# Kernel tuning notes

Measured on AMD Instinct MI355X. Metric: run time of the kernel, lower is better.

## Reference

```python
import jax, jax.numpy as jnp
import numpy as np

B, L, D, H, NL = 16, 256, 768, 12, 4
HD = D // H          # head size = 64; also edge-feature embedding dim
V, E, C, F = 30000, 50, 2, 3072
CLS_ID = 1


def _pos_emb(length, dim):
    # standard sinusoidal positional embedding [L, D]
    pos = jnp.arange(length, dtype=jnp.float32)[:, None]
    div = jnp.exp(-np.log(10000.0) * jnp.arange(0, dim, 2, dtype=jnp.float32) / dim)
    ang = pos * div[None, :]
    pe = jnp.zeros((length, dim), jnp.float32)
    return pe.at[:, 0::2].set(jnp.sin(ang)).at[:, 1::2].set(jnp.cos(ang))


def _ln(x, g, b, eps=1e-5):
    m = x.mean(-1, keepdims=True)
    v = x.var(-1, keepdims=True)
    return (x - m) * jax.lax.rsqrt(v + eps) * g + b


def setup_inputs() -> dict:
    key = jax.random.key(0)
    ks = jax.random.split(key, 16)
    s = 0.02
    word_ids = jax.random.randint(ks[0], (B, L), 0, V).at[:, 0].set(CLS_ID)
    batched_adj = jax.random.bernoulli(ks[1], 0.3, (B, L, L)) | jnp.eye(L, dtype=bool)[None]
    edge_types = jax.random.randint(ks[2], (B, L, L), 0, E)
    word_emb = (jax.random.normal(ks[3], (V, D)) * s).at[0].set(0.0)   # padding_idx=0
    edge_emb = (jax.random.normal(ks[4], (E, HD)) * s).at[0].set(0.0)  # padding_idx=0
    pw = lambda k, shp: jax.random.normal(k, shp) * s
    return {
        "word_ids": word_ids, "batched_adj": batched_adj, "edge_types": edge_types,
        "word_emb": word_emb, "edge_emb": edge_emb,
        "Wq": pw(ks[5], (NL, D, D)), "bq": jnp.zeros((NL, D)),
        "Wk": pw(ks[6], (NL, D, D)), "bk": jnp.zeros((NL, D)),
        "Wv": pw(ks[7], (NL, D, D)), "bv": jnp.zeros((NL, D)),
        "Wo": pw(ks[8], (NL, D, D)), "bo": jnp.zeros((NL, D)),
        "ln1_g": jnp.ones((NL, D)), "ln1_b": jnp.zeros((NL, D)),
        "W1": pw(ks[9], (NL, D, F)), "b1": jnp.zeros((NL, F)),
        "W2": pw(ks[10], (NL, F, D)), "b2": jnp.zeros((NL, D)),
        "ln2_g": jnp.ones((NL, D)), "ln2_b": jnp.zeros((NL, D)),
        "cls_W": pw(ks[11], (D, C)), "cls_b": jnp.zeros((C,)),
    }


def reference(word_ids, batched_adj, edge_types, word_emb, edge_emb,
              Wq, bq, Wk, bk, Wv, bv, Wo, bo, ln1_g, ln1_b,
              W1, b1, W2, b2, ln2_g, ln2_b, cls_W, cls_b):
    # node features: word embedding + positional embedding
    h = word_emb[word_ids] + _pos_emb(L, D)[None]          # [B,L,D]
    scale = 1.0 / np.sqrt(HD)
    eemb = edge_emb[edge_types]                             # [B,L,L,HD] edge key features
    neg = jnp.asarray(-1e9, h.dtype)
    mask = batched_adj[:, None]                             # [B,1,L,L]
    for l in range(NL):
        q = (h @ Wq[l] + bq[l]).reshape(B, L, H, HD)
        k = (h @ Wk[l] + bk[l]).reshape(B, L, H, HD)
        v = (h @ Wv[l] + bv[l]).reshape(B, L, H, HD)
        # scores: node-node + query . edge-key-feature, adjacency-masked
        scores = jnp.einsum('bihd,bjhd->bhij', q, k)
        scores = scores + jnp.einsum('bihd,bijd->bhij', q, eemb)
        scores = jnp.where(mask, scores * scale, neg)
        att = jax.nn.softmax(scores, axis=-1)               # [B,H,L,L]
        out = jnp.einsum('bhij,bjhd->bihd', att, v).reshape(B, L, D)
        h = _ln(h + (out @ Wo[l] + bo[l]), ln1_g[l], ln1_b[l])
        ff = jax.nn.relu(h @ W1[l] + b1[l]) @ W2[l] + b2[l]
        h = _ln(h + ff, ln2_g[l], ln2_b[l])
    cls_h = h[:, 0]                                         # CLS pooling
    logits = cls_h @ cls_W + cls_b                          # [B,C]
    return logits
```

## Files before the change

### kernel.cpp

```cpp
#include <hip/hip_runtime.h>
#include <hip/hip_bf16.h>

#define BB 16
#define LL 256
#define DD 768
#define HH 12
#define HDD 64
#define NLL 4
#define FF 3072
#define EE 50
#define QKVS 2304
#define TOKD ((size_t)BB * LL * DD)

typedef unsigned short ushort_t;
typedef __bf16 bf16x8 __attribute__((ext_vector_type(8)));
typedef float f32x4 __attribute__((ext_vector_type(4)));

__device__ __forceinline__ float b2f(ushort_t u) {
    union { unsigned int i; float f; } x; x.i = ((unsigned int)u) << 16; return x.f;
}
__device__ __forceinline__ ushort_t f2b(float f) {
    unsigned int u = __builtin_bit_cast(unsigned int, f);
    unsigned int r = u + 0x7fffu + ((u >> 16) & 1u);
    return (ushort_t)(r >> 16);
}

__device__ __forceinline__ void gl2lds16(const void* g, void* l) {
    __builtin_amdgcn_global_load_lds(
        (const __attribute__((address_space(1))) unsigned int*)g,
        (__attribute__((address_space(3))) unsigned int*)l,
        16, 0, 0);
}

__global__ __launch_bounds__(256) void transpose_f2b(
    const float* __restrict__ in, ushort_t* __restrict__ out, int R, int C,
    long inZ, long outZ)
{
    __shared__ ushort_t tile[32][33];
    in  += (long)blockIdx.z * inZ;
    out += (long)blockIdx.z * outZ;
    int c0 = blockIdx.x * 32, r0 = blockIdx.y * 32;
    int tx = threadIdx.x, ty = threadIdx.y;
#pragma unroll
    for (int i = 0; i < 32; i += 8)
        tile[ty + i][tx] = f2b(in[(long)(r0 + ty + i) * C + c0 + tx]);
    __syncthreads();
#pragma unroll
    for (int i = 0; i < 32; i += 8)
        out[(long)(c0 + ty + i) * R + r0 + tx] = tile[tx][ty + i];
}

__global__ __launch_bounds__(256) void fuse_bias_kernel(
    const float* __restrict__ bq, const float* __restrict__ bk,
    const float* __restrict__ bv, int l, float* __restrict__ out)
{
    int n = blockIdx.x * 256 + threadIdx.x;
    if (n >= QKVS) return;
    float v = (n < DD) ? bq[l * DD + n]
            : (n < 2 * DD) ? bk[l * DD + n - DD]
            : bv[l * DD + n - 2 * DD];
    out[n] = v;
}

__global__ __launch_bounds__(256) void embed_kernel(
    const int* __restrict__ wids, const float* __restrict__ wemb,
    float* __restrict__ hf, ushort_t* __restrict__ hb)
{
    long idx = (long)blockIdx.x * 256 + threadIdx.x;
    int d = (int)(idx % DD);
    int t = (int)(idx / DD);
    int lpos = t & (LL - 1);
    int wid = wids[t];
    float freq = expf(-9.210340371976184f * (float)(d & ~1) * (1.f / (float)DD));
    float ang = (float)lpos * freq;
    float pe = (d & 1) ? cosf(ang) : sinf(ang);
    float hv = wemb[(long)wid * DD + d] + pe;
    hf[idx] = hv;
    hb[idx] = f2b(hv);
}

__global__ __launch_bounds__(256) void gemm_bf16(
    const ushort_t* __restrict__ A, const ushort_t* __restrict__ Bt,
    const float* __restrict__ bias,
    ushort_t* __restrict__ outb, float* __restrict__ outf,
    int M, int N, int K, int Ksl, int relu)
{
    __shared__ __align__(16) ushort_t As[128 * 32];
    __shared__ __align__(16) ushort_t Bs[128 * 32];
    const int tid = threadIdx.x;
    const int wave = tid >> 6, lane = tid & 63;
    const int quad = lane >> 4, l16 = lane & 15;
    const int m0 = blockIdx.y * 128, n0 = blockIdx.x * 128;
    const int z = blockIdx.z;
    const int kbase = z * Ksl;
    const int wm = (wave >> 1) * 64, wn = (wave & 1) * 64;
    const ushort_t* Ab = A + (long)m0 * K;
    const ushort_t* Bb = Bt + (long)n0 * K;

    f32x4 acc[4][4];
#pragma unroll
    for (int mi = 0; mi < 4; ++mi)
#pragma unroll
        for (int ni = 0; ni < 4; ++ni) acc[mi][ni] = (f32x4){0.f, 0.f, 0.f, 0.f};

    const int nk = Ksl >> 5;
    for (int kt = 0; kt < nk; ++kt) {
        const int k0 = kbase + (kt << 5);
        __syncthreads();
#pragma unroll
        for (int i = 0; i < 2; ++i) {
            int c = tid + i * 256;
            int row = c >> 2, kc = (c & 3) * 8;
            char* la = (char*)As + (wave * 1024 + i * 4096);
            char* lb = (char*)Bs + (wave * 1024 + i * 4096);
            gl2lds16(&Ab[(long)row * K + k0 + kc], la);
            gl2lds16(&Bb[(long)row * K + k0 + kc], lb);
        }
        __syncthreads();
        bf16x8 af[4], bfr[4];
#pragma unroll
        for (int t = 0; t < 4; ++t)
            af[t] = *(const bf16x8*)&As[(wm + t * 16 + l16) * 32 + quad * 8];
#pragma unroll
        for (int t = 0; t < 4; ++t)
            bfr[t] = *(const bf16x8*)&Bs[(wn + t * 16 + l16) * 32 + quad * 8];
#pragma unroll
        for (int mi = 0; mi < 4; ++mi)
#pragma unroll
            for (int ni = 0; ni < 4; ++ni)
                acc[mi][ni] = __builtin_amdgcn_mfma_f32_16x16x32_bf16(
                    af[mi], bfr[ni], acc[mi][ni], 0, 0, 0);
    }

    float* outfz = outf ? outf + (size_t)z * M * N : nullptr;
#pragma unroll
    for (int ni = 0; ni < 4; ++ni) {
        int col = n0 + wn + ni * 16 + l16;
        float bv = (bias && z == 0) ? bias[col] : 0.f;
#pragma unroll
        for (int mi = 0; mi < 4; ++mi) {
#pragma unroll
            for (int r = 0; r < 4; ++r) {
                int row = m0 + wm + mi * 16 + quad * 4 + r;
                float vv = acc[mi][ni][r] + bv;
                if (relu) vv = fmaxf(vv, 0.f);
                if (outb) outb[(long)row * N + col] = f2b(vv);
                if (outfz) outfz[(long)row * N + col] = vv;
            }
        }
    }
}

#define QS_STR 72
#define VT_STR 264
#define P_STR  264
#define S_STR  257
#define PE_STR 53

__global__ __launch_bounds__(256) void attn_kernel(
    const ushort_t* __restrict__ qkv,
    const int* __restrict__ adjm, const int* __restrict__ etyp,
    const float* __restrict__ eemb, ushort_t* __restrict__ out)
{
    __shared__ __align__(16) char smem[64448];
    ushort_t* VT = (ushort_t*)smem;
    float*    S  = (float*)(smem + 33792);
    ushort_t* P  = (ushort_t*)(smem + 50240);
    float*    Pe = (float*)(smem + 58688);
    char*     U  = smem + 62080;
    float* invrow = (float*)(smem + 64384);
    ushort_t* Qs = (ushort_t*)U;
    float*    red = (float*)U;

    const int blk = blockIdx.x;
    const int qt = blk & 15;
    const int h  = (blk >> 4) % HH;
    const int b  = blk / (16 * HH);
    const int i0 = qt * 16;
    const int tid = threadIdx.x;
    const int wave = tid >> 6, lane = tid & 63;
    const int quad = lane >> 4, l16 = lane & 15;

    if (tid < 128) {
        int row = tid >> 3, d0 = (tid & 7) * 8;
        *(int4*)&Qs[row * QS_STR + d0] =
            *(const int4*)&qkv[((long)(b * LL + i0 + row)) * QKVS + h * HDD + d0];
    }
#pragma unroll
    for (int i = 0; i < 8; ++i) {
        int c = tid + i * 256;
        int j = c >> 3, d0 = (c & 7) * 8;
        int4 raw = *(const int4*)&qkv[((long)(b * LL + j)) * QKVS + 2 * DD + h * HDD + d0];
        const ushort_t* vals = (const ushort_t*)&raw;
#pragma unroll
        for (int u = 0; u < 8; ++u) VT[(d0 + u) * VT_STR + j] = vals[u];
    }
    __syncthreads();

    {
        int e = wave * 16 + l16;
        f32x4 acc = (f32x4){0.f, 0.f, 0.f, 0.f};
#pragma unroll
        for (int kk = 0; kk < 2; ++kk) {
            bf16x8 af = *(const bf16x8*)&Qs[l16 * QS_STR + kk * 32 + quad * 8];
            bf16x8 bf = (bf16x8){0, 0, 0, 0, 0, 0, 0, 0};
            if (e < EE) {
                const float* ep = &eemb[(long)e * HDD + kk * 32 + quad * 8];
#pragma unroll
                for (int u = 0; u < 8; ++u) bf[u] = (__bf16)ep[u];
            }
            acc = __builtin_amdgcn_mfma_f32_16x16x32_bf16(af, bf, acc, 0, 0, 0);
        }
        if (e < EE) {
#pragma unroll
            for (int r = 0; r < 4; ++r) Pe[(quad * 4 + r) * PE_STR + e] = acc[r];
        }
    }

#pragma unroll
    for (int jt = 0; jt < 4; ++jt) {
        int jtile = wave * 4 + jt;
        int j = jtile * 16 + l16;
        f32x4 acc = (f32x4){0.f, 0.f, 0.f, 0.f};
#pragma unroll
        for (int kk = 0; kk < 2; ++kk) {
            bf16x8 af = *(const bf16x8*)&Qs[l16 * QS_STR + kk * 32 + quad * 8];
            bf16x8 bf = *(const bf16x8*)&qkv[((long)(b * LL + j)) * QKVS + DD + h * HDD + kk * 32 + quad * 8];
            acc = __builtin_amdgcn_mfma_f32_16x16x32_bf16(af, bf, acc, 0, 0, 0);
        }
#pragma unroll
        for (int r = 0; r < 4; ++r)
            S[(quad * 4 + r) * S_STR + jtile * 16 + l16] = acc[r];
    }
    __syncthreads();

    {
        const int row = tid & 15, seg = tid >> 4;
        const int i = i0 + row;
        const int* etp = etyp + ((long)(b * LL + i)) * LL + seg * 16;
        const int* adp = adjm + ((long)(b * LL + i)) * LL + seg * 16;
        int etv[16], adv[16];
#pragma unroll
        for (int t = 0; t < 4; ++t) {
            *(int4*)&etv[t * 4] = *(const int4*)&etp[t * 4];
            *(int4*)&adv[t * 4] = *(const int4*)&adp[t * 4];
        }
        float vals[16];
        float pmax = -1e30f;
#pragma unroll
        for (int c = 0; c < 16; ++c) {
            float s = S[row * S_STR + seg * 16 + c];
            float pe = Pe[row * PE_STR + etv[c]];
            float vv = adv[c] ? (s + pe) * 0.125f : -1e30f;
            vals[c] = vv;
            pmax = fmaxf(pmax, vv);
        }
        red[row * 17 + seg] = pmax;
        __syncthreads();
        float m = -1e30f;
#pragma unroll
        for (int g = 0; g < 16; ++g) m = fmaxf(m, red[row * 17 + g]);
        float sum = 0.f;
#pragma unroll
        for (int c = 0; c < 16; ++c) {
            float p = __expf(vals[c] - m);
            ushort_t pb = f2b(p);
            sum += b2f(pb);
            P[row * P_STR + seg * 16 + c] = pb;
        }
        red[272 + row * 17 + seg] = sum;
        __syncthreads();
        if (tid < 16) {
            float tot = 0.f;
#pragma unroll
            for (int g = 0; g < 16; ++g) tot += red[272 + tid * 17 + g];
            invrow[tid] = 1.f / tot;
        }
        __syncthreads();
    }

    {
        f32x4 acc = (f32x4){0.f, 0.f, 0.f, 0.f};
#pragma unroll
        for (int kt = 0; kt < 8; ++kt) {
            bf16x8 af = *(const bf16x8*)&P[l16 * P_STR + kt * 32 + quad * 8];
            bf16x8 bf = *(const bf16x8*)&VT[(wave * 16 + l16) * VT_STR + kt * 32 + quad * 8];
            acc = __builtin_amdgcn_mfma_f32_16x16x32_bf16(af, bf, acc, 0, 0, 0);
        }
#pragma unroll
        for (int r = 0; r < 4; ++r) {
            int row = quad * 4 + r;
            float ov = acc[r] * invrow[row];
            out[((long)(b * LL + i0 + row)) * DD + h * HDD + wave * 16 + l16] = f2b(ov);
        }
    }
}

__global__ __launch_bounds__(256) void ln_kernel(
    float* __restrict__ hf, ushort_t* __restrict__ hb,
    const float* __restrict__ proj, int nparts,
    const float* __restrict__ g, const float* __restrict__ be)
{
    const int r = blockIdx.x, tid = threadIdx.x;
    const long rb = (long)r * DD;
    float x[3];
#pragma unroll
    for (int i = 0; i < 3; ++i) {
        int d = tid + i * 256;
        float t = hf[rb + d];
        for (int p = 0; p < nparts; ++p) t += proj[(size_t)p * TOKD + rb + d];
        x[i] = t;
    }
    float s = x[0] + x[1] + x[2];
    float s2 = x[0] * x[0] + x[1] * x[1] + x[2] * x[2];
#pragma unroll
    for (int o = 1; o < 64; o <<= 1) { s += __shfl_xor(s, o); s2 += __shfl_xor(s2, o); }
    __shared__ float rs[4], rq[4];
    int wave = tid >> 6;
    if ((tid & 63) == 0) { rs[wave] = s; rq[wave] = s2; }
    __syncthreads();
    float S  = rs[0] + rs[1] + rs[2] + rs[3];
    float S2 = rq[0] + rq[1] + rq[2] + rq[3];
    float mean = S * (1.f / (float)DD);
    float var  = S2 * (1.f / (float)DD) - mean * mean;
    float rstd = rsqrtf(var + 1e-5f);
#pragma unroll
    for (int i = 0; i < 3; ++i) {
        int d = tid + i * 256;
        float y = (x[i] - mean) * rstd * g[d] + be[d];
        hf[rb + d] = y;
        hb[rb + d] = f2b(y);
    }
}

__global__ __launch_bounds__(256) void cls_kernel(
    const float* __restrict__ hf, const float* __restrict__ W,
    const float* __restrict__ bias, float* __restrict__ out)
{
    int b = blockIdx.x, tid = threadIdx.x;
    const float* hr = hf + (long)b * LL * DD;
    float p0 = 0.f, p1 = 0.f;
    for (int d = tid; d < DD; d += 256) {
        float hv = hr[d];
        p0 = fmaf(hv, W[d * 2 + 0], p0);
        p1 = fmaf(hv, W[d * 2 + 1], p1);
    }
#pragma unroll
    for (int o = 1; o < 64; o <<= 1) { p0 += __shfl_xor(p0, o); p1 += __shfl_xor(p1, o); }
    __shared__ float r0[4], r1[4];
    int wave = tid >> 6;
    if ((tid & 63) == 0) { r0[wave] = p0; r1[wave] = p1; }
    __syncthreads();
    if (tid == 0) {
        out[b * 2 + 0] = r0[0] + r0[1] + r0[2] + r0[3] + bias[0];
        out[b * 2 + 1] = r1[0] + r1[1] + r1[2] + r1[3] + bias[1];
    }
}

extern "C" void kernel_launch(void* const* d_in, const int* in_sizes, int n_in,
                              void* d_out, int out_size, void* d_ws, size_t ws_size,
                              hipStream_t stream)
{
    const int* word_ids = (const int*)d_in[0];
    const int* adjm     = (const int*)d_in[1];
    const int* etyp     = (const int*)d_in[2];
    const float* wemb   = (const float*)d_in[3];
    const float* eemb   = (const float*)d_in[4];
    const float* Wq     = (const float*)d_in[5];
    const float* bq     = (const float*)d_in[6];
    const float* Wk     = (const float*)d_in[7];
    const float* bk     = (const float*)d_in[8];
    const float* Wv     = (const float*)d_in[9];
    const float* bv     = (const float*)d_in[10];
    const float* Wo     = (const float*)d_in[11];
    const float* bo     = (const float*)d_in[12];
    const float* ln1g   = (const float*)d_in[13];
    const float* ln1b   = (const float*)d_in[14];
    const float* W1     = (const float*)d_in[15];
    const float* b1     = (const float*)d_in[16];
    const float* W2     = (const float*)d_in[17];
    const float* b2     = (const float*)d_in[18];
    const float* ln2g   = (const float*)d_in[19];
    const float* ln2b   = (const float*)d_in[20];
    const float* clsW   = (const float*)d_in[21];
    const float* clsb   = (const float*)d_in[22];
    float* outp = (float*)d_out;

    char* ws = (char*)d_ws;
    size_t off = 0;
    auto alloc = [&](size_t bytes) -> char* {
        char* p = ws + off;
        off += (bytes + 255) & ~(size_t)255;
        return p;
    };
    const size_t DxD = (size_t)DD * DD;
    const size_t DxF = (size_t)DD * FF;
    const size_t TOK = (size_t)BB * LL;
    const size_t LSTR = (size_t)QKVS * DD + DxD + 2 * DxF;

    float*    hf  = (float*)alloc(TOK * DD * 4);
    ushort_t* hb  = (ushort_t*)alloc(TOK * DD * 2);
    ushort_t* qkv = (ushort_t*)alloc(TOK * QKVS * 2);
    ushort_t* ao  = (ushort_t*)alloc(TOK * DD * 2);
    float*    pjf = (float*)alloc(TOK * DD * 4);
    ushort_t* tw  = (ushort_t*)alloc(DxF * 2);
    ushort_t* ff1 = qkv;
    size_t tier1 = off + TOK * DD * 4;
    size_t tier2 = tier1 + 2 * TOK * DD * 4;
    size_t tier3 = tier2 + NLL * LSTR * 2;
    int S_o = 1, S_f = 1;
    ushort_t* cache = nullptr;
    if (ws_size >= tier1) { (void)alloc(TOK * DD * 4); S_o = 2; S_f = 2; }
    if (ws_size >= tier2) { (void)alloc(2 * TOK * DD * 4); S_f = 4; }
    if (ws_size >= tier3) { cache = (ushort_t*)alloc(NLL * LSTR * 2); }
    (void)in_sizes; (void)n_in; (void)out_size;

    dim3 tb(32, 8, 1);
    if (cache) {
        transpose_f2b<<<dim3(24, 24, NLL), tb, 0, stream>>>(Wq, cache,                 DD, DD, DxD, LSTR);
        transpose_f2b<<<dim3(24, 24, NLL), tb, 0, stream>>>(Wk, cache + DD * DD,       DD, DD, DxD, LSTR);
        transpose_f2b<<<dim3(24, 24, NLL), tb, 0, stream>>>(Wv, cache + 2 * DD * DD,   DD, DD, DxD, LSTR);
        transpose_f2b<<<dim3(24, 24, NLL), tb, 0, stream>>>(Wo, cache + 3 * DD * DD,   DD, DD, DxD, LSTR);
        transpose_f2b<<<dim3(96, 24, NLL), tb, 0, stream>>>(W1, cache + 4 * DD * DD,   DD, FF, DxF, LSTR);
        transpose_f2b<<<dim3(24, 96, NLL), tb, 0, stream>>>(W2, cache + 4 * DD * DD + DxF, FF, DD, DxF, LSTR);
    }

    embed_kernel<<<(int)(TOK * DD / 256), 256, 0, stream>>>(word_ids, wemb, hf, hb);

    const int M = (int)TOK;
    for (int l = 0; l < NLL; ++l) {
        const ushort_t *BtQKV, *BtO, *BtW1, *BtW2;
        if (cache) {
            const ushort_t* base = cache + (size_t)l * LSTR;
            BtQKV = base; BtO = base + 3 * DD * DD;
            BtW1 = base + 4 * DD * DD; BtW2 = base + 4 * DD * DD + DxF;
        } else {
            BtQKV = tw; BtO = tw; BtW1 = tw; BtW2 = tw;
        }
        fuse_bias_kernel<<<9, 256, 0, stream>>>(bq, bk, bv, l, pjf);
        if (!cache) {
            transpose_f2b<<<dim3(24, 24), tb, 0, stream>>>(Wq + (size_t)l * DxD, tw,               DD, DD, 0, 0);
            transpose_f2b<<<dim3(24, 24), tb, 0, stream>>>(Wk + (size_t)l * DxD, tw + DD * DD,     DD, DD, 0, 0);
            transpose_f2b<<<dim3(24, 24), tb, 0, stream>>>(Wv + (size_t)l * DxD, tw + 2 * DD * DD, DD, DD, 0, 0);
        }
        gemm_bf16<<<dim3(QKVS / 128, M / 128, 1), 256, 0, stream>>>(
            hb, BtQKV, pjf, qkv, nullptr, M, QKVS, DD, DD, 0);
        attn_kernel<<<BB * HH * 16, 256, 0, stream>>>(qkv, adjm, etyp, eemb, ao);
        if (!cache)
            transpose_f2b<<<dim3(24, 24), tb, 0, stream>>>(Wo + (size_t)l * DxD, tw, DD, DD, 0, 0);
        gemm_bf16<<<dim3(DD / 128, M / 128, S_o), 256, 0, stream>>>(
            ao, BtO, bo + l * DD, nullptr, pjf, M, DD, DD, DD / S_o, 0);
        ln_kernel<<<M, 256, 0, stream>>>(hf, hb, pjf, S_o, ln1g + l * DD, ln1b + l * DD);
        if (!cache)
            transpose_f2b<<<dim3(96, 24), tb, 0, stream>>>(W1 + (size_t)l * DxF, tw, DD, FF, 0, 0);
        gemm_bf16<<<dim3(FF / 128, M / 128, 1), 256, 0, stream>>>(
            hb, BtW1, b1 + l * FF, ff1, nullptr, M, FF, DD, DD, 1);
        if (!cache)
            transpose_f2b<<<dim3(24, 96), tb, 0, stream>>>(W2 + (size_t)l * DxF, tw, FF, DD, 0, 0);
        gemm_bf16<<<dim3(DD / 128, M / 128, S_f), 256, 0, stream>>>(
            ff1, BtW2, b2 + l * DD, nullptr, pjf, M, DD, FF, FF / S_f, 0);
        ln_kernel<<<M, 256, 0, stream>>>(hf, hb, pjf, S_f, ln2g + l * DD, ln2b + l * DD);
    }
    cls_kernel<<<BB, 256, 0, stream>>>(hf, clsW, clsb, outp);
}
```

Baseline: 1.248 ms.

## Triple-buffer GEMM LDS tiles with async prefetch two stages ahead

```diff
diff --git a/kernel.cpp b/kernel.cpp
--- a/kernel.cpp
+++ b/kernel.cpp
@@ -85,8 +85,8 @@
     ushort_t* __restrict__ outb, float* __restrict__ outf,
     int M, int N, int K, int Ksl, int relu)
 {
-    __shared__ __align__(16) ushort_t As[128 * 32];
-    __shared__ __align__(16) ushort_t Bs[128 * 32];
+    __shared__ __align__(16) ushort_t As[3][128 * 32];
+    __shared__ __align__(16) ushort_t Bs[3][128 * 32];
     const int tid = threadIdx.x;
     const int wave = tid >> 6, lane = tid & 63;
     const int quad = lane >> 4, l16 = lane & 15;
@@ -97,6 +97,8 @@
     const ushort_t* Ab = A + (long)m0 * K;
     const ushort_t* Bb = Bt + (long)n0 * K;
 
+    const int srow = tid >> 2, skc = (tid & 3) * 8;
+
     f32x4 acc[4][4];
 #pragma unroll
     for (int mi = 0; mi < 4; ++mi)
@@ -104,32 +106,49 @@
         for (int ni = 0; ni < 4; ++ni) acc[mi][ni] = (f32x4){0.f, 0.f, 0.f, 0.f};
 
     const int nk = Ksl >> 5;
+
+    auto stage = [&](int kt, ushort_t* Ad, ushort_t* Bd) {
+        const int k0 = kbase + (kt << 5);
+        const ushort_t* ga = &Ab[(long)srow * K + k0 + skc];
+        const ushort_t* gb = &Bb[(long)srow * K + k0 + skc];
+        char* la = (char*)Ad + wave * 1024;
+        char* lb = (char*)Bd + wave * 1024;
+        gl2lds16(ga, la);
+        gl2lds16(gb, lb);
+        gl2lds16(ga + (long)64 * K, la + 4096);
+        gl2lds16(gb + (long)64 * K, lb + 4096);
+    };
+
+    ushort_t *A0 = As[0], *A1 = As[1], *A2 = As[2];
+    ushort_t *B0 = Bs[0], *B1 = Bs[1], *B2 = Bs[2];
+
+    stage(0, A0, B0);
+    stage(1, A1, B1);
+
     for (int kt = 0; kt < nk; ++kt) {
-        const int k0 = kbase + (kt << 5);
-        __syncthreads();
-#pragma unroll
-        for (int i = 0; i < 2; ++i) {
-            int c = tid + i * 256;
-            int row = c >> 2, kc = (c & 3) * 8;
-            char* la = (char*)As + (wave * 1024 + i * 4096);
-            char* lb = (char*)Bs + (wave * 1024 + i * 4096);
-            gl2lds16(&Ab[(long)row * K + k0 + kc], la);
-            gl2lds16(&Bb[(long)row * K + k0 + kc], lb);
-        }
-        __syncthreads();
+        if (kt + 1 < nk) {
+            asm volatile("s_waitcnt vmcnt(4)" ::: "memory");
+        } else {
+            asm volatile("s_waitcnt vmcnt(0)" ::: "memory");
+        }
+        __builtin_amdgcn_s_barrier();
+        __builtin_amdgcn_sched_barrier(0);
+        if (kt + 2 < nk) stage(kt + 2, A2, B2);
         bf16x8 af[4], bfr[4];
 #pragma unroll
         for (int t = 0; t < 4; ++t)
-            af[t] = *(const bf16x8*)&As[(wm + t * 16 + l16) * 32 + quad * 8];
+            af[t] = *(const bf16x8*)&A0[(wm + t * 16 + l16) * 32 + quad * 8];
 #pragma unroll
         for (int t = 0; t < 4; ++t)
-            bfr[t] = *(const bf16x8*)&Bs[(wn + t * 16 + l16) * 32 + quad * 8];
+            bfr[t] = *(const bf16x8*)&B0[(wn + t * 16 + l16) * 32 + quad * 8];
 #pragma unroll
         for (int mi = 0; mi < 4; ++mi)
 #pragma unroll
             for (int ni = 0; ni < 4; ++ni)
                 acc[mi][ni] = __builtin_amdgcn_mfma_f32_16x16x32_bf16(
                     af[mi], bfr[ni], acc[mi][ni], 0, 0, 0);
+        ushort_t* ta = A0; A0 = A1; A1 = A2; A2 = ta;
+        ushort_t* tb = B0; B0 = B1; B1 = B2; B2 = tb;
     }
 
     float* outfz = outf ? outf + (size_t)z * M * N : nullptr;
```

New measurement: 1.213 ms. 1.03x faster.
